# Performance work log

Measured on AMD Instinct MI355X. Metric: run time of the kernel, lower is better.

The kernel has to match this reference:

```python
import jax, jax.numpy as jnp
import numpy as np

# Dimensions (match init_kwargs / input_specs)
B, CIN, COUT = 4, 8, 32
HIN, WIN = 721, 1440      # input (nlat, nlon)
HOUT, WOUT = 361, 720     # output (nlat, nlon)
K = 9                     # morlet basis: kernel_shape[0]*kernel_shape[1]
NNZ = 32                  # nonzeros per (basis fn, output-lat) row of sparse psi
PSCALE = WIN // WOUT      # longitudinal downsampling factor (must be integer)


def setup_inputs() -> dict:
    key = jax.random.key(0)
    k1, k2, k3, k4, k5 = jax.random.split(key, 5)
    x = jax.random.normal(k1, (B, CIN, HIN, WIN), jnp.float32)
    # Localized sparse support: input lat rows near the matching output lat
    # (emulates the theta_cutoff neighborhood of the precomputed DISCO tensor).
    base_row = jnp.round(jnp.arange(HOUT) * (HIN - 1) / (HOUT - 1)).astype(jnp.int32)
    drow = jax.random.randint(k2, (K, HOUT, NNZ), -2, 3)
    rows = jnp.clip(base_row[None, :, None] + drow, 0, HIN - 1)
    # small longitudinal offsets; the contraction shifts them over all output lons
    cols = jax.random.randint(k3, (K, HOUT, NNZ), 0, 16)
    psi_idx = (rows * WIN + cols).astype(jnp.int32)          # [K, HOUT, NNZ]
    psi_vals = jax.random.normal(k4, (K, HOUT, NNZ), jnp.float32) / NNZ
    weight = jax.random.normal(k5, (COUT, CIN, K), jnp.float32) / np.sqrt(CIN * K)
    return {"x": x, "psi_idx": psi_idx, "psi_vals": psi_vals, "weight": weight}


def _disco_conv(x, psi_idx, psi_vals, weight):
    # DISCO S2 contraction (dense math of torch_harmonics _disco_s2_contraction):
    #   out[b,o,xo,po] = sum_{c,k} weight[o,c,k] * y[b,c,k,xo,po]
    Bv, C, Hin, Win = x.shape
    rows = psi_idx // Win               # [K, Hout, NNZ]
    cols = psi_idx % Win
    x_flat = x.reshape(Bv, C, Hin * Win)

    def step(_, po):
        cols_p = (cols + po * PSCALE) % Win
        idx = rows * Win + cols_p                        # [K,Hout,NNZ]
        xg = x_flat[:, :, idx]                           # [B,C,K,Hout,NNZ] gather
        y_po = jnp.einsum('bckxn,kxn->bckx', xg, psi_vals)
        return None, y_po

    _, y = jax.lax.scan(step, None, jnp.arange(WOUT))    # [Wout,B,C,K,Hout]
    out = jnp.einsum('pbckx,ock->boxp', y, weight)       # [B,Cout,Hout,Wout]
    return out


def reference(x, psi_idx, psi_vals, weight):
    # The wrapper only casts to float32 around the conv; inputs are already fp32.
    return _disco_conv(x.astype(jnp.float32), psi_idx, psi_vals, weight)
```

## Files before the change

### kernel.cpp

```cpp
#include <hip/hip_runtime.h>
#include <hip/hip_bf16.h>

#define HIN   721
#define WIN   1440
#define HOUT_ 361
#define WOUT_ 720
#define NB    4
#define CIN_  8
#define COUT_ 32
#define KT    9
#define NNZ_  32

typedef short  bsh8   __attribute__((ext_vector_type(8)));
typedef float  f32x16 __attribute__((ext_vector_type(16)));
typedef unsigned int u32x4 __attribute__((ext_vector_type(4)));

static __device__ __forceinline__ unsigned short f2bf(float f) {
  unsigned u = __builtin_bit_cast(unsigned, f);
  u += 0x7fffu + ((u >> 16) & 1u);
  return (unsigned short)(u >> 16);
}

static __device__ __forceinline__ unsigned pack2(float a, float b) {
  __hip_bfloat162 h = __float22bfloat162_rn(make_float2(a, b));
  unsigned u; __builtin_memcpy(&u, &h, 4);
  return u;
}

__global__ __launch_bounds__(256) void coeff_kernel(
    const int*   __restrict__ psi_idx,
    const float* __restrict__ psi_vals,
    const float* __restrict__ weight,
    unsigned short* __restrict__ Cg)
{
  __shared__ float Cl[256 * 81];
  __shared__ float wl[COUT_ * CIN_ * KT];
  __shared__ float S[KT][80];

  const int x = blockIdx.x, tid = threadIdx.x;

  for (int i = tid; i < KT * 80; i += 256) ((float*)S)[i] = 0.f;
  for (int i = tid; i < COUT_ * CIN_ * KT; i += 256) wl[i] = weight[i];
  __syncthreads();

  for (int i = tid; i < KT * NNZ_; i += 256) {
    int k = i >> 5, n = i & 31;
    int gi  = (k * HOUT_ + x) * NNZ_ + n;
    int idx = psi_idx[gi];
    int r   = idx / WIN;
    int col = idx - r * WIN;
    int s   = r - 2 * x + 2;
    int slot = (s * 2 + (col & 1)) * 8 + (col >> 1);
    atomicAdd(&S[k][slot], psi_vals[gi]);
  }
  __syncthreads();

  {
    const float* wrow = &wl[tid * KT];
    float w[KT];
    #pragma unroll
    for (int k = 0; k < KT; ++k) w[k] = wrow[k];
    float* seg = &Cl[tid * 81];
    #pragma unroll
    for (int slot = 0; slot < 80; ++slot) {
      float acc = 0.f;
      #pragma unroll
      for (int k = 0; k < KT; ++k) acc += w[k] * S[k][slot];
      seg[slot] = acc;
    }
  }
  __syncthreads();

  for (int chunk = tid; chunk < 8 * 10 * 32; chunk += 256) {
    int j   = chunk / 320;
    int rem = chunk - j * 320;
    int qb  = rem >> 5, o = rem & 31;
    u32x4 pack;
    #pragma unroll
    for (int h = 0; h < 4; ++h) {
      int q0 = qb * 8 + 2 * h;
      int c0 = q0 / 10, ql0 = q0 - c0 * 10;
      int q1 = q0 + 1;
      int c1 = q1 / 10, ql1 = q1 - c1 * 10;
      unsigned lo = f2bf(Cl[(o * CIN_ + c0) * 81 + ql0 * 8 + j]);
      unsigned hi = f2bf(Cl[(o * CIN_ + c1) * 81 + ql1 * 8 + j]);
      pack[h] = lo | (hi << 16);
    }
    *(u32x4*)&Cg[((size_t)x * 2560 + (size_t)((j * 10 + qb) * 32 + o)) * 8] = pack;
  }
}

#define PB   128
#define ROWS 136
#define RST  256

__global__ __launch_bounds__(256, 4) void disco_main_kernel(
    const float* __restrict__ x,
    const unsigned short* __restrict__ Cg,
    float* __restrict__ out)
{
  __shared__ __align__(16) unsigned char Ut[ROWS * RST];

  const int g   = blockIdx.x;
  const int xcd = g & 7, lin = g >> 3;
  const int swz = xcd * 1083 + lin;
  const int xo  = swz / 24;
  const int rem = swz - xo * 24;
  const int pt  = rem % 6;
  const int b   = rem / 6;
  const int p0  = pt * PB;
  const int tid = threadIdx.x;

  const float* xb = x + (size_t)b * (CIN_ * HIN * WIN);

  int rr[5];
  #pragma unroll
  for (int s = 0; s < 5; ++s) {
    int r = 2 * xo + s - 2;
    rr[s] = r < 0 ? 0 : (r > HIN - 1 ? HIN - 1 : r);
  }

  {
    float4 v[2][4];
    #pragma unroll
    for (int pass = 0; pass < 2; ++pass) {
      const int u  = tid + pass * 256;
      const int ch = u / 68, rp = u - ch * 68;
      int cw = p0 + 2 * rp; if (cw >= WOUT_) cw -= WOUT_;
      #pragma unroll
      for (int m = 0; m < 4; ++m) {
        int qp = 4 * ch + m;
        int c  = (qp * 205) >> 10;
        int s  = qp - c * 5;
        v[pass][m] = *(const float4*)&xb[(size_t)(c * HIN + rr[s]) * WIN + 2 * cw];
      }
    }
    #pragma unroll
    for (int pass = 0; pass < 2; ++pass) {
      const int u  = tid + pass * 256;
      const int ch = u / 68, rp = u - ch * 68;
      u32x4 lo, hi;
      #pragma unroll
      for (int m = 0; m < 4; ++m) {
        lo[m] = pack2(v[pass][m].x, v[pass][m].y);
        hi[m] = pack2(v[pass][m].z, v[pass][m].w);
      }
      const int byte0 = rp * 512 + ((ch ^ (rp & 7)) << 4);
      *(u32x4*)&Ut[byte0]       = lo;
      *(u32x4*)&Ut[byte0 + RST] = hi;
    }
    if (tid < 168) {
      const int u  = 512 + tid;
      const int ch = u / 68, rp = u - ch * 68;
      int cw = p0 + 2 * rp; if (cw >= WOUT_) cw -= WOUT_;
      float4 w[4];
      #pragma unroll
      for (int m = 0; m < 4; ++m) {
        int qp = 4 * ch + m;
        int c  = (qp * 205) >> 10;
        int s  = qp - c * 5;
        w[m] = *(const float4*)&xb[(size_t)(c * HIN + rr[s]) * WIN + 2 * cw];
      }
      u32x4 lo, hi;
      #pragma unroll
      for (int m = 0; m < 4; ++m) {
        lo[m] = pack2(w[m].x, w[m].y);
        hi[m] = pack2(w[m].z, w[m].w);
      }
      const int byte0 = rp * 512 + ((ch ^ (rp & 7)) << 4);
      *(u32x4*)&Ut[byte0]       = lo;
      *(u32x4*)&Ut[byte0 + RST] = hi;
    }
  }
  __syncthreads();

  const int lane = tid & 63;
  const int wv   = tid >> 6;
  const int half = lane >> 5;
  const int l31  = lane & 31;

  const unsigned short* cgx = Cg + (size_t)xo * 2560 * 8
                                 + (size_t)(half * 32 + l31) * 8;

  bsh8 a_cur[5], a_nxt[5];
  #pragma unroll
  for (int kb = 0; kb < 5; ++kb)
    a_cur[kb] = *(const bsh8*)&cgx[kb * 512];

  f32x16 acc = {};

  #pragma unroll
  for (int j = 0; j < 8; ++j) {
    if (j < 7) {
      #pragma unroll
      for (int kb = 0; kb < 5; ++kb)
        a_nxt[kb] = *(const bsh8*)&cgx[(j + 1) * 2560 + kb * 512];
    }
    const int row   = wv * 32 + l31 + j;
    const int rbase = row * RST;
    const int rsh   = (row >> 1) & 7;
    #pragma unroll
    for (int kb = 0; kb < 5; ++kb) {
      bsh8 bfrag = *(const bsh8*)&Ut[rbase + (((2 * kb + half) ^ rsh) << 4)];
      acc = __builtin_amdgcn_mfma_f32_32x32x16_bf16(a_cur[kb], bfrag, acc, 0, 0, 0);
    }
    #pragma unroll
    for (int kb = 0; kb < 5; ++kb) a_cur[kb] = a_nxt[kb];
  }

  const int p = p0 + wv * 32 + l31;
  if (p < WOUT_) {
    #pragma unroll
    for (int r = 0; r < 16; ++r) {
      int o = (r & 3) + 8 * (r >> 2) + 4 * half;
      __builtin_nontemporal_store(
          acc[r], &out[((size_t)(b * COUT_ + o) * HOUT_ + xo) * WOUT_ + p]);
    }
  }
}

extern "C" void kernel_launch(void* const* d_in, const int* in_sizes, int n_in,
                              void* d_out, int out_size, void* d_ws, size_t ws_size,
                              hipStream_t stream) {
  const float* x        = (const float*)d_in[0];
  const int*   psi_idx  = (const int*)d_in[1];
  const float* psi_vals = (const float*)d_in[2];
  const float* weight   = (const float*)d_in[3];
  float* out = (float*)d_out;
  unsigned short* Cg = (unsigned short*)d_ws;

  coeff_kernel<<<dim3(HOUT_), 256, 0, stream>>>(psi_idx, psi_vals, weight, Cg);
  disco_main_kernel<<<dim3(6 * NB * HOUT_), 256, 0, stream>>>(x, Cg, out);
}
```

Before: 97.72 us.

## Double output-longitude tile per block with two accumulators per wave

```diff
diff --git a/kernel.cpp b/kernel.cpp
--- a/kernel.cpp
+++ b/kernel.cpp
@@ -90,11 +90,11 @@
   }
 }
 
-#define PB   128
-#define ROWS 136
-#define RST  256
-
-__global__ __launch_bounds__(256, 4) void disco_main_kernel(
+#define PB   256
+#define ROWS 264
+#define RST  192
+
+__global__ __launch_bounds__(256, 3) void disco_main_kernel(
     const float* __restrict__ x,
     const unsigned short* __restrict__ Cg,
     float* __restrict__ out)
@@ -103,119 +103,142 @@
 
   const int g   = blockIdx.x;
   const int xcd = g & 7, lin = g >> 3;
-  const int swz = xcd * 1083 + lin;
-  const int xo  = swz / 24;
-  const int rem = swz - xo * 24;
-  const int pt  = rem % 6;
-  const int b   = rem / 6;
+  const int swz = (xcd < 4) ? xcd * 542 + lin : 4 * 542 + (xcd - 4) * 541 + lin;
+  const int xo  = swz / 12;
+  const int rem = swz - xo * 12;
+  const int pt  = rem % 3;
+  const int b   = rem / 3;
   const int p0  = pt * PB;
   const int tid = threadIdx.x;
-
-  const float* xb = x + (size_t)b * (CIN_ * HIN * WIN);
-
-  int rr[5];
-  #pragma unroll
-  for (int s = 0; s < 5; ++s) {
-    int r = 2 * xo + s - 2;
-    rr[s] = r < 0 ? 0 : (r > HIN - 1 ? HIN - 1 : r);
-  }
-
-  {
-    float4 v[2][4];
-    #pragma unroll
-    for (int pass = 0; pass < 2; ++pass) {
-      const int u  = tid + pass * 256;
-      const int ch = u / 68, rp = u - ch * 68;
-      int cw = p0 + 2 * rp; if (cw >= WOUT_) cw -= WOUT_;
-      #pragma unroll
-      for (int m = 0; m < 4; ++m) {
-        int qp = 4 * ch + m;
-        int c  = (qp * 205) >> 10;
-        int s  = qp - c * 5;
-        v[pass][m] = *(const float4*)&xb[(size_t)(c * HIN + rr[s]) * WIN + 2 * cw];
-      }
-    }
-    #pragma unroll
-    for (int pass = 0; pass < 2; ++pass) {
-      const int u  = tid + pass * 256;
-      const int ch = u / 68, rp = u - ch * 68;
-      u32x4 lo, hi;
-      #pragma unroll
-      for (int m = 0; m < 4; ++m) {
-        lo[m] = pack2(v[pass][m].x, v[pass][m].y);
-        hi[m] = pack2(v[pass][m].z, v[pass][m].w);
-      }
-      const int byte0 = rp * 512 + ((ch ^ (rp & 7)) << 4);
-      *(u32x4*)&Ut[byte0]       = lo;
-      *(u32x4*)&Ut[byte0 + RST] = hi;
-    }
-    if (tid < 168) {
-      const int u  = 512 + tid;
-      const int ch = u / 68, rp = u - ch * 68;
-      int cw = p0 + 2 * rp; if (cw >= WOUT_) cw -= WOUT_;
-      float4 w[4];
-      #pragma unroll
-      for (int m = 0; m < 4; ++m) {
-        int qp = 4 * ch + m;
-        int c  = (qp * 205) >> 10;
-        int s  = qp - c * 5;
-        w[m] = *(const float4*)&xb[(size_t)(c * HIN + rr[s]) * WIN + 2 * cw];
-      }
-      u32x4 lo, hi;
-      #pragma unroll
-      for (int m = 0; m < 4; ++m) {
-        lo[m] = pack2(w[m].x, w[m].y);
-        hi[m] = pack2(w[m].z, w[m].w);
-      }
-      const int byte0 = rp * 512 + ((ch ^ (rp & 7)) << 4);
-      *(u32x4*)&Ut[byte0]       = lo;
-      *(u32x4*)&Ut[byte0 + RST] = hi;
-    }
-  }
-  __syncthreads();
 
   const int lane = tid & 63;
   const int wv   = tid >> 6;
   const int half = lane >> 5;
   const int l31  = lane & 31;
+  const int wbase = wv * 64;
 
   const unsigned short* cgx = Cg + (size_t)xo * 2560 * 8
                                  + (size_t)(half * 32 + l31) * 8;
 
-  bsh8 a_cur[5], a_nxt[5];
+  bsh8 a_cur[5];
   #pragma unroll
   for (int kb = 0; kb < 5; ++kb)
     a_cur[kb] = *(const bsh8*)&cgx[kb * 512];
 
-  f32x16 acc = {};
+  const float* xb = x + (size_t)b * (CIN_ * HIN * WIN);
+
+  int rr[5];
+  #pragma unroll
+  for (int s = 0; s < 5; ++s) {
+    int r = 2 * xo + s - 2;
+    rr[s] = r < 0 ? 0 : (r > HIN - 1 ? HIN - 1 : r);
+  }
+
+  #pragma unroll
+  for (int bp = 0; bp < 2; ++bp) {
+    float4 v0[4], v1[4];
+    const int uA = tid + (2 * bp) * 256, uB = uA + 256;
+    const int chA = uA / 132, rpA = uA - chA * 132;
+    const int chB = uB / 132, rpB = uB - chB * 132;
+    int cwA = p0 + 2 * rpA; if (cwA >= WOUT_) cwA -= WOUT_;
+    int cwB = p0 + 2 * rpB; if (cwB >= WOUT_) cwB -= WOUT_;
+    #pragma unroll
+    for (int m = 0; m < 4; ++m) {
+      int qpA = 4 * chA + m, cA = (qpA * 205) >> 10, sA = qpA - cA * 5;
+      v0[m] = *(const float4*)&xb[(size_t)(cA * HIN + rr[sA]) * WIN + 2 * cwA];
+      int qpB = 4 * chB + m, cB = (qpB * 205) >> 10, sB = qpB - cB * 5;
+      v1[m] = *(const float4*)&xb[(size_t)(cB * HIN + rr[sB]) * WIN + 2 * cwB];
+    }
+    u32x4 lo, hi;
+    #pragma unroll
+    for (int m = 0; m < 4; ++m) { lo[m] = pack2(v0[m].x, v0[m].y); hi[m] = pack2(v0[m].z, v0[m].w); }
+    int byte0 = (2 * rpA) * RST + ((chA ^ (rpA & 3)) << 4);
+    *(u32x4*)&Ut[byte0]       = lo;
+    *(u32x4*)&Ut[byte0 + RST] = hi;
+    #pragma unroll
+    for (int m = 0; m < 4; ++m) { lo[m] = pack2(v1[m].x, v1[m].y); hi[m] = pack2(v1[m].z, v1[m].w); }
+    byte0 = (2 * rpB) * RST + ((chB ^ (rpB & 3)) << 4);
+    *(u32x4*)&Ut[byte0]       = lo;
+    *(u32x4*)&Ut[byte0 + RST] = hi;
+  }
+  {
+    const int uA = tid + 1024;
+    const int chA = uA / 132, rpA = uA - chA * 132;
+    int cwA = p0 + 2 * rpA; if (cwA >= WOUT_) cwA -= WOUT_;
+    float4 v0[4], v1[4];
+    int chB = 0, rpB = 0;
+    const bool tail = tid < 40;
+    if (tail) {
+      const int uB = tid + 1280;
+      chB = uB / 132; rpB = uB - chB * 132;
+    }
+    int cwB = p0 + 2 * rpB; if (cwB >= WOUT_) cwB -= WOUT_;
+    #pragma unroll
+    for (int m = 0; m < 4; ++m) {
+      int qpA = 4 * chA + m, cA = (qpA * 205) >> 10, sA = qpA - cA * 5;
+      v0[m] = *(const float4*)&xb[(size_t)(cA * HIN + rr[sA]) * WIN + 2 * cwA];
+    }
+    if (tail) {
+      #pragma unroll
+      for (int m = 0; m < 4; ++m) {
+        int qpB = 4 * chB + m, cB = (qpB * 205) >> 10, sB = qpB - cB * 5;
+        v1[m] = *(const float4*)&xb[(size_t)(cB * HIN + rr[sB]) * WIN + 2 * cwB];
+      }
+    }
+    u32x4 lo, hi;
+    #pragma unroll
+    for (int m = 0; m < 4; ++m) { lo[m] = pack2(v0[m].x, v0[m].y); hi[m] = pack2(v0[m].z, v0[m].w); }
+    int byte0 = (2 * rpA) * RST + ((chA ^ (rpA & 3)) << 4);
+    *(u32x4*)&Ut[byte0]       = lo;
+    *(u32x4*)&Ut[byte0 + RST] = hi;
+    if (tail) {
+      #pragma unroll
+      for (int m = 0; m < 4; ++m) { lo[m] = pack2(v1[m].x, v1[m].y); hi[m] = pack2(v1[m].z, v1[m].w); }
+      byte0 = (2 * rpB) * RST + ((chB ^ (rpB & 3)) << 4);
+      *(u32x4*)&Ut[byte0]       = lo;
+      *(u32x4*)&Ut[byte0 + RST] = hi;
+    }
+  }
+  __syncthreads();
+
+  f32x16 acc0 = {};
+  f32x16 acc1 = {};
 
   #pragma unroll
   for (int j = 0; j < 8; ++j) {
+    bsh8 a_nxt[5];
     if (j < 7) {
       #pragma unroll
       for (int kb = 0; kb < 5; ++kb)
         a_nxt[kb] = *(const bsh8*)&cgx[(j + 1) * 2560 + kb * 512];
     }
-    const int row   = wv * 32 + l31 + j;
-    const int rbase = row * RST;
-    const int rsh   = (row >> 1) & 7;
+    const int row0 = wbase + l31 + j;
+    const int row1 = row0 + 32;
+    const int rb0  = row0 * RST, f0 = (row0 >> 1) & 3;
+    const int rb1  = row1 * RST, f1 = (row1 >> 1) & 3;
     #pragma unroll
     for (int kb = 0; kb < 5; ++kb) {
-      bsh8 bfrag = *(const bsh8*)&Ut[rbase + (((2 * kb + half) ^ rsh) << 4)];
-      acc = __builtin_amdgcn_mfma_f32_32x32x16_bf16(a_cur[kb], bfrag, acc, 0, 0, 0);
-    }
-    #pragma unroll
-    for (int kb = 0; kb < 5; ++kb) a_cur[kb] = a_nxt[kb];
-  }
-
-  const int p = p0 + wv * 32 + l31;
-  if (p < WOUT_) {
-    #pragma unroll
-    for (int r = 0; r < 16; ++r) {
-      int o = (r & 3) + 8 * (r >> 2) + 4 * half;
-      __builtin_nontemporal_store(
-          acc[r], &out[((size_t)(b * COUT_ + o) * HOUT_ + xo) * WOUT_ + p]);
-    }
+      const int ch = 2 * kb + half;
+      bsh8 b0 = *(const bsh8*)&Ut[rb0 + ((ch ^ f0) << 4)];
+      acc0 = __builtin_amdgcn_mfma_f32_32x32x16_bf16(a_cur[kb], b0, acc0, 0, 0, 0);
+      bsh8 b1 = *(const bsh8*)&Ut[rb1 + ((ch ^ f1) << 4)];
+      acc1 = __builtin_amdgcn_mfma_f32_32x32x16_bf16(a_cur[kb], b1, acc1, 0, 0, 0);
+    }
+    if (j < 7) {
+      #pragma unroll
+      for (int kb = 0; kb < 5; ++kb) a_cur[kb] = a_nxt[kb];
+    }
+  }
+
+  const int p = p0 + wbase + l31;
+  #pragma unroll
+  for (int r = 0; r < 16; ++r) {
+    int o = (r & 3) + 8 * (r >> 2) + 4 * half;
+    size_t base = ((size_t)(b * COUT_ + o) * HOUT_ + xo) * WOUT_;
+    if (p < WOUT_)
+      __builtin_nontemporal_store(acc0[r], &out[base + p]);
+    if (p + 32 < WOUT_)
+      __builtin_nontemporal_store(acc1[r], &out[base + p + 32]);
   }
 }
 
@@ -230,5 +253,5 @@
   unsigned short* Cg = (unsigned short*)d_ws;
 
   coeff_kernel<<<dim3(HOUT_), 256, 0, stream>>>(psi_idx, psi_vals, weight, Cg);
-  disco_main_kernel<<<dim3(6 * NB * HOUT_), 256, 0, stream>>>(x, Cg, out);
-}
+  disco_main_kernel<<<dim3(3 * NB * HOUT_), 256, 0, stream>>>(x, Cg, out);
+}
```

Result: no change. 96.27 us (-1.5%).
